# Kernel tuning notes

Hardware: AMD Instinct MI355X
Metric: run time of the kernel (lower is better)

The kernel has to match this reference:

```python
import jax, jax.numpy as jnp
from jax import lax
import numpy as np

B = 2048; IMG = 28; K = 3; CIN = 1; HC = 32; LC = 16; WID = 64; HID = 64
LIS = IMG - 3 * (K - 1)           # 22: latent image size
FLAT = LIS * LIS * HC             # 15488
BLK = WID * LC                    # 1024: hypernet block size
T1 = 10.0; T0 = 0.0; NSTEP = 20   # fixed-step RK4 replaces adaptive dopri5
VAR = 0.1                         # p_z0 diagonal covariance


def _conv(x, w, b):  # w: [Cout,Cin,k,k], VALID conv, stride 1
    y = lax.conv_general_dilated(x, w, (1, 1), 'VALID',
                                 dimension_numbers=('NCHW', 'OIHW', 'NCHW'))
    return y + b[None, :, None, None]


def _convT(x, w, b):  # w: [Cin,Cout,k,k] (pytorch ConvTranspose2d layout)
    wf = jnp.flip(w, (2, 3)).transpose(1, 0, 2, 3)  # -> OIHW, spatially flipped
    y = lax.conv_general_dilated(x, wf, (1, 1), [(K - 1, K - 1), (K - 1, K - 1)],
                                 dimension_numbers=('NCHW', 'OIHW', 'NCHW'))
    return y + b[None, :, None, None]


def _forward(x, c0w, c0b, c1w, c1b, c2w, c2b, elw, elb, dlw, dlb,
             t0w, t0b, t1w, t1b, t2w, t2b, h1w, h1b, h2w, h2b, h3w, h3b):
    # ---- encoder (dropout in eval = identity) ----
    h = jnp.tanh(_conv(x, c0w, c0b))
    h = jnp.tanh(_conv(h, c1w, c1b))
    h = jnp.tanh(_conv(h, c2w, c2b))
    z1 = h.reshape(h.shape[0], -1) @ elw + elb          # [B, LC]
    # ---- decoder ----
    d = jnp.tanh(z1 @ dlw + dlb)                         # [B, FLAT]
    d = d.reshape(-1, HC, LIS, LIS)
    d = jnp.tanh(_convT(d, t0w, t0b))
    d = jnp.tanh(_convT(d, t1w, t1b))
    recon = _convT(d, t2w, t2b)                          # [B, CIN, 28, 28]

    # ---- CNF vector field with analytic trace ----
    def hyper(t):
        p = jnp.tanh(jnp.reshape(jnp.asarray(t, jnp.float32), (1, 1)) @ h1w + h1b)
        p = jnp.tanh(p @ h2w + h2b)
        p = (p @ h3w + h3b).reshape(-1)
        W = p[:BLK].reshape(WID, LC)
        U = p[BLK:2 * BLK].reshape(WID, LC) * jax.nn.sigmoid(p[2 * BLK:3 * BLK].reshape(WID, LC))
        Bb = p[3 * BLK:]                                 # [WID]
        return W, Bb, U

    def f(t, z):
        W, Bb, U = hyper(t)
        hh = jnp.tanh(jnp.einsum('bd,wd->wb', z, W) + Bb[:, None])   # [WID, B]
        dz = jnp.einsum('wb,wd->bd', hh, U) / WID                     # [B, LC]
        s = jnp.sum(W * U, axis=1)                                    # [WID]: sum_i W_w[i]U_w[i]
        tr = jnp.mean((1.0 - hh * hh) * s[:, None], axis=0)           # [B] analytic trace
        return dz, -tr[:, None]

    dt = (T0 - T1) / NSTEP

    def step(state, i):
        z, lp = state
        t = T1 + i * dt
        k1z, k1l = f(t, z)
        k2z, k2l = f(t + 0.5 * dt, z + 0.5 * dt * k1z)
        k3z, k3l = f(t + 0.5 * dt, z + 0.5 * dt * k2z)
        k4z, k4l = f(t + dt, z + dt * k3z)
        z = z + dt / 6.0 * (k1z + 2 * k2z + 2 * k3z + k4z)
        lp = lp + dt / 6.0 * (k1l + 2 * k2l + 2 * k3l + k4l)
        return (z, lp), None

    lp1 = jnp.zeros((z1.shape[0], 1), z1.dtype)
    (z0, lp0), _ = lax.scan(step, (z1, lp1), jnp.arange(NSTEP, dtype=jnp.float32))

    # MultivariateNormal(0, 0.1*I) log_prob
    logp = -0.5 * (LC * jnp.log(2 * jnp.pi) + LC * jnp.log(VAR) + jnp.sum(z0 * z0, -1) / VAR)
    x_probs = jnp.mean(logp - lp0[:, 0])
    return recon, x_probs


def setup_inputs() -> dict:
    key = jax.random.key(0)
    ks = jax.random.split(key, 16)
    n = jax.random.normal
    s = jnp.float32(0.05)
    z = jnp.zeros
    OUT3 = 3 * BLK + WID
    return {
        'x': n(ks[0], (B, CIN, IMG, IMG), jnp.float32),
        'c0w': n(ks[1], (HC, CIN, K, K)) * s, 'c0b': z((HC,)),
        'c1w': n(ks[2], (HC, HC, K, K)) * s, 'c1b': z((HC,)),
        'c2w': n(ks[3], (HC, HC, K, K)) * s, 'c2b': z((HC,)),
        'elw': n(ks[4], (FLAT, LC)) * s, 'elb': z((LC,)),
        'dlw': n(ks[5], (LC, FLAT)) * s, 'dlb': z((FLAT,)),
        't0w': n(ks[6], (HC, HC, K, K)) * s, 't0b': z((HC,)),
        't1w': n(ks[7], (HC, HC, K, K)) * s, 't1b': z((HC,)),
        't2w': n(ks[8], (HC, CIN, K, K)) * s, 't2b': z((CIN,)),
        'h1w': n(ks[9], (1, HID)) * s, 'h1b': z((HID,)),
        'h2w': n(ks[10], (HID, HID)) * s, 'h2b': z((HID,)),
        'h3w': n(ks[11], (HID, OUT3)) * s, 'h3b': z((OUT3,)),
    }


def reference(x, c0w, c0b, c1w, c1b, c2w, c2b, elw, elb, dlw, dlb,
              t0w, t0b, t1w, t1b, t2w, t2b, h1w, h1b, h2w, h2b, h3w, h3b):
    return _forward(x, c0w, c0b, c1w, c1b, c2w, c2b, elw, elb, dlw, dlb,
                    t0w, t0b, t1w, t1b, t2w, t2b, h1w, h1b, h2w, h2b, h3w, h3b)
```

## Files before the change

### kernel.cpp

```cpp
#include <hip/hip_runtime.h>
#include <math.h>

#define Bsz 2048

using bf16x8 = __attribute__((ext_vector_type(8))) short;
using f32x4  = __attribute__((ext_vector_type(4))) float;

__device__ __forceinline__ float fast_tanh(float x){
    float e = __expf(2.0f * x);
    return 1.0f - 2.0f / (e + 1.0f);
}
__device__ __forceinline__ float fast_sigmoid(float x){
    return 1.0f / (1.0f + __expf(-x));
}
__device__ __forceinline__ unsigned short f2b(float f){
    union { float f; unsigned u; } v; v.f = f;
    unsigned r = v.u + 0x7FFFu + ((v.u >> 16) & 1u);
    return (unsigned short)(r >> 16);
}
__device__ __forceinline__ float b2f(unsigned short s){
    union { unsigned u; float f; } v; v.u = ((unsigned)s) << 16;
    return v.f;
}

__device__ __forceinline__ float stage_t(int sidx){
    int i  = sidx >> 2, st = sidx & 3;
    float t = 10.0f - 0.5f * (float)i;
    if (st == 1 || st == 2) t -= 0.25f;
    else if (st == 3)       t -= 0.5f;
    return t;
}

__global__ void k_prep(const float* __restrict__ c1w, const float* __restrict__ c2w,
                       const float* __restrict__ t0w, const float* __restrict__ t1w,
                       const float* __restrict__ elw, const float* __restrict__ dlw,
                       const float* __restrict__ elb, const float* __restrict__ dlb,
                       unsigned short* __restrict__ wc1, unsigned short* __restrict__ wc2,
                       unsigned short* __restrict__ wt0, unsigned short* __restrict__ wt1,
                       unsigned short* __restrict__ elwT, unsigned short* __restrict__ dlwT,
                       float* __restrict__ dlbT, float* __restrict__ z1, int full){
    int gsz = gridDim.x * 256;
    for (int i = blockIdx.x*256 + threadIdx.x; i < 9216; i += gsz){
        int ci = i & 31, co = (i >> 5) & 31, s = i >> 10;
        wc1[i] = f2b(c1w[(co*32 + ci)*9 + s]);
        wc2[i] = f2b(c2w[(co*32 + ci)*9 + s]);
        wt0[i] = f2b(t0w[(ci*32 + co)*9 + (8 - s)]);
        wt1[i] = f2b(t1w[(ci*32 + co)*9 + (8 - s)]);
    }
    if (!full) return;
    for (int i = blockIdx.x*256 + threadIdx.x; i < 32768; i += gsz)
        z1[i] = elb[i & 15];
    for (int i = blockIdx.x*256 + threadIdx.x; i < 15488; i += gsz){
        int pos = i >> 5, ci = i & 31;
        dlbT[i] = dlb[ci*484 + pos];
    }
    for (int i = blockIdx.x*256 + threadIdx.x; i < 247808; i += gsz){
        int l = i / 15488, f2 = i - l*15488;
        int pos = f2 >> 5, ci = f2 & 31;
        elwT[i] = f2b(elw[(ci*484 + pos)*16 + l]);
    }
    for (int i = blockIdx.x*256 + threadIdx.x; i < 247808; i += gsz){
        int f2 = i >> 4, l = i & 15;
        int pos = f2 >> 5, ci = f2 & 31;
        dlwT[i] = f2b(dlw[l*15488 + ci*484 + pos]);
    }
}

__global__ void __launch_bounds__(256)
k_enc01(const float* __restrict__ x, const float* __restrict__ c0w,
        const float* __restrict__ c0b, const unsigned short* __restrict__ wc1,
        const float* __restrict__ c1b, unsigned short* __restrict__ A1,
        int cb){
    __shared__ __align__(16) unsigned short A0L[676*40];
    const int tid = threadIdx.x, b = blockIdx.x;
    const float* xin = x + (size_t)(cb + b)*784;

    for (int pos = tid; pos < 676; pos += 256){
        int y = pos / 26, xx = pos - y*26;
        float v[9];
#pragma unroll
        for (int r = 0; r < 3; r++)
#pragma unroll
            for (int s = 0; s < 3; s++)
                v[r*3+s] = xin[(y+r)*28 + xx + s];
        unsigned short* ob = A0L + pos*40;
#pragma unroll
        for (int g = 0; g < 8; g++){
            float a0 = c0b[g*4+0], a1 = c0b[g*4+1], a2 = c0b[g*4+2], a3 = c0b[g*4+3];
#pragma unroll
            for (int k = 0; k < 9; k++){
                a0 += v[k] * c0w[(g*4+0)*9 + k];
                a1 += v[k] * c0w[(g*4+1)*9 + k];
                a2 += v[k] * c0w[(g*4+2)*9 + k];
                a3 += v[k] * c0w[(g*4+3)*9 + k];
            }
            ushort4 o;
            o.x = f2b(fast_tanh(a0)); o.y = f2b(fast_tanh(a1));
            o.z = f2b(fast_tanh(a2)); o.w = f2b(fast_tanh(a3));
            *(ushort4*)(ob + g*4) = o;
        }
    }
    __syncthreads();

    const int wave = tid >> 6, lane = tid & 63;
    const int q = lane >> 4, nn = lane & 15;
    bf16x8 af[2][9];
#pragma unroll
    for (int mt = 0; mt < 2; mt++)
#pragma unroll
        for (int s = 0; s < 9; s++)
            af[mt][s] = *(const bf16x8*)(wc1 + s*1024 + (mt*16 + nn)*32 + q*8);
    float4 bc0 = *(const float4*)(c1b + q*4);
    float4 bc1 = *(const float4*)(c1b + 16 + q*4);
    unsigned short* outb = A1 + (size_t)b*25088;

    for (int t = wave; t < 36; t += 4){
        int pos = t*16 + nn;
        int oy = pos / 24, ox = pos - oy*24;
        const unsigned short* ib = A0L + (oy*26 + ox)*40 + q*8;
        f32x4 acc0 = {0.f,0.f,0.f,0.f}, acc1 = {0.f,0.f,0.f,0.f};
#pragma unroll
        for (int r = 0; r < 3; r++){
            bf16x8 b0 = *(const bf16x8*)(ib + (r*26 + 0)*40);
            bf16x8 b1 = *(const bf16x8*)(ib + (r*26 + 1)*40);
            bf16x8 b2 = *(const bf16x8*)(ib + (r*26 + 2)*40);
            acc0 = __builtin_amdgcn_mfma_f32_16x16x32_bf16(af[0][r*3+0], b0, acc0, 0,0,0);
            acc1 = __builtin_amdgcn_mfma_f32_16x16x32_bf16(af[1][r*3+0], b0, acc1, 0,0,0);
            acc0 = __builtin_amdgcn_mfma_f32_16x16x32_bf16(af[0][r*3+1], b1, acc0, 0,0,0);
            acc1 = __builtin_amdgcn_mfma_f32_16x16x32_bf16(af[1][r*3+1], b1, acc1, 0,0,0);
            acc0 = __builtin_amdgcn_mfma_f32_16x16x32_bf16(af[0][r*3+2], b2, acc0, 0,0,0);
            acc1 = __builtin_amdgcn_mfma_f32_16x16x32_bf16(af[1][r*3+2], b2, acc1, 0,0,0);
        }
        int opix = oy*24 + ox;
        ushort4 o0, o1;
        o0.x = f2b(fast_tanh(acc0[0] + bc0.x)); o0.y = f2b(fast_tanh(acc0[1] + bc0.y));
        o0.z = f2b(fast_tanh(acc0[2] + bc0.z)); o0.w = f2b(fast_tanh(acc0[3] + bc0.w));
        o1.x = f2b(fast_tanh(acc1[0] + bc1.x)); o1.y = f2b(fast_tanh(acc1[1] + bc1.y));
        o1.z = f2b(fast_tanh(acc1[2] + bc1.z)); o1.w = f2b(fast_tanh(acc1[3] + bc1.w));
        *(ushort4*)(outb + opix*32 + q*4)      = o0;
        *(ushort4*)(outb + opix*32 + 16 + q*4) = o1;
    }
}

template<int IL, int OL, int OW, int OOFF, int INS, int OUTS>
__global__ void __launch_bounds__(256)
k_convM(const unsigned short* __restrict__ in, const unsigned short* __restrict__ wg,
        const float* __restrict__ bias, unsigned short* __restrict__ out, int CH){
    constexpr int N  = OL * OL;
    constexpr int NT = (N + 15) / 16;
    const int tid = threadIdx.x;
    const int wave = tid >> 6, lane = tid & 63;
    const int q = lane >> 4, nn = lane & 15;
    const int nw = gridDim.x * 4;

    bf16x8 af[2][9];
#pragma unroll
    for (int mt = 0; mt < 2; mt++)
#pragma unroll
        for (int s = 0; s < 9; s++)
            af[mt][s] = *(const bf16x8*)(wg + s*1024 + (mt*16 + nn)*32 + q*8);
    float4 bc0 = *(const float4*)(bias + q*4);
    float4 bc1 = *(const float4*)(bias + 16 + q*4);

    for (int t = blockIdx.x*4 + wave; t < CH*NT; t += nw){
        int img = t / NT, tt = t - img*NT;
        const unsigned short* inb = in + (size_t)img * INS;
        unsigned short* outb = out + (size_t)img * OUTS;
        int pos = tt*16 + nn;
        int pc  = pos < N ? pos : N - 1;
        int oy = pc / OL, ox = pc - oy*OL;
        const unsigned short* ib = inb + (oy*IL + ox)*32 + q*8;
        f32x4 acc0 = {0.f,0.f,0.f,0.f}, acc1 = {0.f,0.f,0.f,0.f};
#pragma unroll
        for (int r = 0; r < 3; r++){
            bf16x8 b0 = *(const bf16x8*)(ib + (r*IL + 0)*32);
            bf16x8 b1 = *(const bf16x8*)(ib + (r*IL + 1)*32);
            bf16x8 b2 = *(const bf16x8*)(ib + (r*IL + 2)*32);
            acc0 = __builtin_amdgcn_mfma_f32_16x16x32_bf16(af[0][r*3+0], b0, acc0, 0,0,0);
            acc1 = __builtin_amdgcn_mfma_f32_16x16x32_bf16(af[1][r*3+0], b0, acc1, 0,0,0);
            acc0 = __builtin_amdgcn_mfma_f32_16x16x32_bf16(af[0][r*3+1], b1, acc0, 0,0,0);
            acc1 = __builtin_amdgcn_mfma_f32_16x16x32_bf16(af[1][r*3+1], b1, acc1, 0,0,0);
            acc0 = __builtin_amdgcn_mfma_f32_16x16x32_bf16(af[0][r*3+2], b2, acc0, 0,0,0);
            acc1 = __builtin_amdgcn_mfma_f32_16x16x32_bf16(af[1][r*3+2], b2, acc1, 0,0,0);
        }
        if (pos < N){
            int opix = oy*OW + ox + OOFF;
            ushort4 o0, o1;
            o0.x = f2b(fast_tanh(acc0[0] + bc0.x)); o0.y = f2b(fast_tanh(acc0[1] + bc0.y));
            o0.z = f2b(fast_tanh(acc0[2] + bc0.z)); o0.w = f2b(fast_tanh(acc0[3] + bc0.w));
            o1.x = f2b(fast_tanh(acc1[0] + bc1.x)); o1.y = f2b(fast_tanh(acc1[1] + bc1.y));
            o1.z = f2b(fast_tanh(acc1[2] + bc1.z)); o1.w = f2b(fast_tanh(acc1[3] + bc1.w));
            *(ushort4*)(outb + opix*32 + q*4)      = o0;
            *(ushort4*)(outb + opix*32 + 16 + q*4) = o1;
        }
    }
}

__global__ void __launch_bounds__(256)
k_encg(const unsigned short* __restrict__ A2, const unsigned short* __restrict__ elwT,
       float* __restrict__ z1, int cb, int CH){
    int wave = threadIdx.x >> 6, lane = threadIdx.x & 63;
    int q = lane >> 4, nn = lane & 15;
    int imgb = blockIdx.x*16;
    const unsigned short* ap = A2 + (size_t)(imgb + nn)*15488 + q*8;
    const unsigned short* bp = elwT + (size_t)nn*15488 + q*8;
    f32x4 acc = {0.f,0.f,0.f,0.f};
    int s0 = blockIdx.y*121;
#pragma unroll 2
    for (int s = s0 + wave; s < s0 + 121; s += 4){
        bf16x8 a = *(const bf16x8*)(ap + s*32);
        bf16x8 b = *(const bf16x8*)(bp + s*32);
        acc = __builtin_amdgcn_mfma_f32_16x16x32_bf16(a, b, acc, 0,0,0);
    }
    float* zp = z1 + (size_t)(cb + imgb)*16;
#pragma unroll
    for (int i = 0; i < 4; i++)
        atomicAdd(zp + (q*4 + i)*16 + nn, acc[i]);
}

__global__ void __launch_bounds__(256)
k_dect0(const float* __restrict__ z1, const unsigned short* __restrict__ dlwT,
        const float* __restrict__ dlbT, const unsigned short* __restrict__ wt0,
        const float* __restrict__ t0b, unsigned short* __restrict__ D1, int cb){
    __shared__ __align__(16) unsigned short D0L[676*40];
    const int tid = threadIdx.x, b = blockIdx.x;
    unsigned short* d1b = D1 + (size_t)b*25088;

    {
        uint4 zq = {0,0,0,0};
        for (int p = tid; p < 676; p += 256){
            int y = p / 26, xx = p - y*26;
            if (y < 2 || y >= 24 || xx < 2 || xx >= 24){
                uint4* pt = (uint4*)(D0L + p*40);
                pt[0] = zq; pt[1] = zq; pt[2] = zq; pt[3] = zq;
            }
        }
        for (int p = tid; p < 784; p += 256){
            int y = p / 28, xx = p - y*28;
            if (y < 2 || y >= 26 || xx < 2 || xx >= 26){
                uint4* pt = (uint4*)(d1b + p*32);
                pt[0] = zq; pt[1] = zq; pt[2] = zq; pt[3] = zq;
            }
        }
    }
    float zz[16];
#pragma unroll
    for (int l = 0; l < 16; l++) zz[l] = z1[(size_t)(cb + b)*16 + l];
    {
        int ci = tid & 31, po = tid >> 5;
#pragma unroll 2
        for (int rr = 0; rr < 61; rr++){
            int pos = rr*8 + po;
            if (pos < 484){
                int y = pos / 22, xx = pos - y*22;
                const unsigned short* w = dlwT + (size_t)(pos*32 + ci)*16;
                bf16x8 w0 = *(const bf16x8*)(w);
                bf16x8 w1 = *(const bf16x8*)(w + 8);
                float a = dlbT[pos*32 + ci];
#pragma unroll
                for (int j = 0; j < 8; j++){
                    a += zz[j]     * b2f((unsigned short)w0[j]);
                    a += zz[8 + j] * b2f((unsigned short)w1[j]);
                }
                D0L[((y+2)*26 + xx + 2)*40 + ci] = f2b(fast_tanh(a));
            }
        }
    }
    __syncthreads();

    const int wave = tid >> 6, lane = tid & 63;
    const int q = lane >> 4, nn = lane & 15;
    bf16x8 af[2][9];
#pragma unroll
    for (int mt = 0; mt < 2; mt++)
#pragma unroll
        for (int s = 0; s < 9; s++)
            af[mt][s] = *(const bf16x8*)(wt0 + s*1024 + (mt*16 + nn)*32 + q*8);
    float4 bc0 = *(const float4*)(t0b + q*4);
    float4 bc1 = *(const float4*)(t0b + 16 + q*4);

    for (int t = wave; t < 36; t += 4){
        int pos = t*16 + nn;
        int oy = pos / 24, ox = pos - oy*24;
        const unsigned short* ib = D0L + (oy*26 + ox)*40 + q*8;
        f32x4 acc0 = {0.f,0.f,0.f,0.f}, acc1 = {0.f,0.f,0.f,0.f};
#pragma unroll
        for (int r = 0; r < 3; r++){
            bf16x8 b0 = *(const bf16x8*)(ib + (r*26 + 0)*40);
            bf16x8 b1 = *(const bf16x8*)(ib + (r*26 + 1)*40);
            bf16x8 b2 = *(const bf16x8*)(ib + (r*26 + 2)*40);
            acc0 = __builtin_amdgcn_mfma_f32_16x16x32_bf16(af[0][r*3+0], b0, acc0, 0,0,0);
            acc1 = __builtin_amdgcn_mfma_f32_16x16x32_bf16(af[1][r*3+0], b0, acc1, 0,0,0);
            acc0 = __builtin_amdgcn_mfma_f32_16x16x32_bf16(af[0][r*3+1], b1, acc0, 0,0,0);
            acc1 = __builtin_amdgcn_mfma_f32_16x16x32_bf16(af[1][r*3+1], b1, acc1, 0,0,0);
            acc0 = __builtin_amdgcn_mfma_f32_16x16x32_bf16(af[0][r*3+2], b2, acc0, 0,0,0);
            acc1 = __builtin_amdgcn_mfma_f32_16x16x32_bf16(af[1][r*3+2], b2, acc1, 0,0,0);
        }
        int opix = oy*28 + ox + 58;
        ushort4 o0, o1;
        o0.x = f2b(fast_tanh(acc0[0] + bc0.x)); o0.y = f2b(fast_tanh(acc0[1] + bc0.y));
        o0.z = f2b(fast_tanh(acc0[2] + bc0.z)); o0.w = f2b(fast_tanh(acc0[3] + bc0.w));
        o1.x = f2b(fast_tanh(acc1[0] + bc1.x)); o1.y = f2b(fast_tanh(acc1[1] + bc1.y));
        o1.z = f2b(fast_tanh(acc1[2] + bc1.z)); o1.w = f2b(fast_tanh(acc1[3] + bc1.w));
        *(ushort4*)(d1b + opix*32 + q*4)      = o0;
        *(ushort4*)(d1b + opix*32 + 16 + q*4) = o1;
    }
}

__global__ void __launch_bounds__(256)
k_dect12(const unsigned short* __restrict__ D1, const unsigned short* __restrict__ wt1,
         const float* __restrict__ t1b, const float* __restrict__ t2w,
         const float* __restrict__ t2b, float* __restrict__ out, int cb){
    __shared__ __align__(16) unsigned short D2L[676*40];
    const int tid = threadIdx.x, b = blockIdx.x;
    const unsigned short* d1b = D1 + (size_t)b*25088;
    const int wave = tid >> 6, lane = tid & 63;
    const int q = lane >> 4, nn = lane & 15;

    bf16x8 af[2][9];
#pragma unroll
    for (int mt = 0; mt < 2; mt++)
#pragma unroll
        for (int s = 0; s < 9; s++)
            af[mt][s] = *(const bf16x8*)(wt1 + s*1024 + (mt*16 + nn)*32 + q*8);
    float4 bc0 = *(const float4*)(t1b + q*4);
    float4 bc1 = *(const float4*)(t1b + 16 + q*4);

    for (int t = wave; t < 43; t += 4){
        int pos = t*16 + nn;
        int pc  = pos < 676 ? pos : 675;
        int oy = pc / 26, ox = pc - oy*26;
        const unsigned short* ib = d1b + (oy*28 + ox)*32 + q*8;
        f32x4 acc0 = {0.f,0.f,0.f,0.f}, acc1 = {0.f,0.f,0.f,0.f};
#pragma unroll
        for (int r = 0; r < 3; r++){
            bf16x8 b0 = *(const bf16x8*)(ib + (r*28 + 0)*32);
            bf16x8 b1 = *(const bf16x8*)(ib + (r*28 + 1)*32);
            bf16x8 b2 = *(const bf16x8*)(ib + (r*28 + 2)*32);
            acc0 = __builtin_amdgcn_mfma_f32_16x16x32_bf16(af[0][r*3+0], b0, acc0, 0,0,0);
            acc1 = __builtin_amdgcn_mfma_f32_16x16x32_bf16(af[1][r*3+0], b0, acc1, 0,0,0);
            acc0 = __builtin_amdgcn_mfma_f32_16x16x32_bf16(af[0][r*3+1], b1, acc0, 0,0,0);
            acc1 = __builtin_amdgcn_mfma_f32_16x16x32_bf16(af[1][r*3+1], b1, acc1, 0,0,0);
            acc0 = __builtin_amdgcn_mfma_f32_16x16x32_bf16(af[0][r*3+2], b2, acc0, 0,0,0);
            acc1 = __builtin_amdgcn_mfma_f32_16x16x32_bf16(af[1][r*3+2], b2, acc1, 0,0,0);
        }
        if (pos < 676){
            int opix = oy*26 + ox;
            ushort4 o0, o1;
            o0.x = f2b(fast_tanh(acc0[0] + bc0.x)); o0.y = f2b(fast_tanh(acc0[1] + bc0.y));
            o0.z = f2b(fast_tanh(acc0[2] + bc0.z)); o0.w = f2b(fast_tanh(acc0[3] + bc0.w));
            o1.x = f2b(fast_tanh(acc1[0] + bc1.x)); o1.y = f2b(fast_tanh(acc1[1] + bc1.y));
            o1.z = f2b(fast_tanh(acc1[2] + bc1.z)); o1.w = f2b(fast_tanh(acc1[3] + bc1.w));
            *(ushort4*)(D2L + opix*40 + q*4)      = o0;
            *(ushort4*)(D2L + opix*40 + 16 + q*4) = o1;
        }
    }
    __syncthreads();

    for (int o = tid; o < 784; o += 256){
        int y = o / 28, xx = o - y*28;
        float a = t2b[0];
#pragma unroll
        for (int r = 0; r < 3; r++){
            int iy = y + r - 2;
            if ((unsigned)iy >= 26u) continue;
#pragma unroll
            for (int s = 0; s < 3; s++){
                int ix = xx + s - 2;
                if ((unsigned)ix >= 26u) continue;
                const unsigned short* pp = D2L + (iy*26 + ix)*40;
                int wi = (2-r)*3 + (2-s);
#pragma unroll
                for (int g = 0; g < 4; g++){
                    bf16x8 h = *(const bf16x8*)(pp + g*8);
#pragma unroll
                    for (int j = 0; j < 8; j++)
                        a += b2f((unsigned short)h[j]) * t2w[(g*8+j)*9 + wi];
                }
            }
        }
        out[(size_t)(cb + b)*784 + o] = a;
    }
}

template<int LOUT, int INW, int OUTW, int OUTOFF>
__device__ __forceinline__ void conv_gemm(const unsigned short* __restrict__ Wg,
                                          const float* __restrict__ bias,
                                          const unsigned short* inL,
                                          unsigned short* outL, int tid){
    constexpr int N  = LOUT * LOUT;
    constexpr int NT = (N + 15) / 16;
    const int lane  = tid & 63;
    const int wave  = tid >> 6;
    const int mtile = wave & 1;
    const int quad  = lane >> 4;
    const int nn    = lane & 15;
    bf16x8 afr[9];
    const unsigned short* wp = Wg + (mtile*16 + nn)*32 + quad*8;
#pragma unroll
    for (int s = 0; s < 9; s++)
        afr[s] = *(const bf16x8*)(wp + s*1024);
    float4 bco = *(const float4*)(bias + mtile*16 + quad*4);
    for (int t = (wave >> 1); t < NT; t += 2){
        int pos = t*16 + nn;
        int pc  = pos < N ? pos : N - 1;
        int y = pc / LOUT, x = pc - y*LOUT;
        const unsigned short* ib = inL + (y*INW + x)*32 + quad*8;
        f32x4 acc = {0.f, 0.f, 0.f, 0.f};
#pragma unroll
        for (int r = 0; r < 3; r++)
#pragma unroll
            for (int s = 0; s < 3; s++)
                acc = __builtin_amdgcn_mfma_f32_16x16x32_bf16(
                        afr[r*3+s], *(const bf16x8*)(ib + (r*INW + s)*32), acc, 0, 0, 0);
        if (pos < N){
            ushort4 o;
            o.x = f2b(fast_tanh(acc[0] + bco.x));
            o.y = f2b(fast_tanh(acc[1] + bco.y));
            o.z = f2b(fast_tanh(acc[2] + bco.z));
            o.w = f2b(fast_tanh(acc[3] + bco.w));
            int opix = y*OUTW + x + OUTOFF;
            *(ushort4*)(outL + opix*32 + mtile*16 + quad*4) = o;
        }
    }
}

__global__ void __launch_bounds__(256)
k_enc_f(const float* __restrict__ x,
        const float* __restrict__ c0w, const float* __restrict__ c0b,
        const unsigned short* __restrict__ wc1, const float* __restrict__ c1b,
        const unsigned short* __restrict__ wc2, const float* __restrict__ c2b,
        const float* __restrict__ elw, const float* __restrict__ elb,
        float* __restrict__ z1){
    __shared__ float X[784];
    __shared__ __align__(16) unsigned short H0[21632];
    __shared__ __align__(16) unsigned short H1[18432];
    __shared__ __align__(16) unsigned short H2[15488];
    __shared__ float red[16*17];
    const int tid = threadIdx.x, b = blockIdx.x;
    for (int i = tid; i < 784; i += 256) X[i] = x[b*784 + i];
    __syncthreads();
    for (int pos = tid; pos < 676; pos += 256){
        int y = pos / 26, xx = pos - y*26;
        float v[9];
#pragma unroll
        for (int r = 0; r < 3; r++)
#pragma unroll
            for (int s = 0; s < 3; s++)
                v[r*3+s] = X[(y+r)*28 + xx + s];
#pragma unroll
        for (int g = 0; g < 8; g++){
            float a0 = c0b[g*4+0], a1 = c0b[g*4+1], a2 = c0b[g*4+2], a3 = c0b[g*4+3];
#pragma unroll
            for (int k = 0; k < 9; k++){
                a0 += v[k] * c0w[(g*4+0)*9 + k];
                a1 += v[k] * c0w[(g*4+1)*9 + k];
                a2 += v[k] * c0w[(g*4+2)*9 + k];
                a3 += v[k] * c0w[(g*4+3)*9 + k];
            }
            ushort4 o;
            o.x = f2b(fast_tanh(a0)); o.y = f2b(fast_tanh(a1));
            o.z = f2b(fast_tanh(a2)); o.w = f2b(fast_tanh(a3));
            *(ushort4*)(H0 + pos*32 + g*4) = o;
        }
    }
    __syncthreads();
    conv_gemm<24, 26, 24, 0>(wc1, c1b, H0, H1, tid);
    __syncthreads();
    conv_gemm<22, 24, 22, 0>(wc2, c2b, H1, H2, tid);
    __syncthreads();
    {
        int fg = tid >> 4, l = tid & 15;
        float a = 0.f;
        for (int ci = 0; ci < 32; ci++)
            for (int pos = fg; pos < 484; pos += 16)
                a += b2f(H2[pos*32 + ci]) * elw[(ci*484 + pos)*16 + l];
        red[fg*17 + l] = a;
        __syncthreads();
        if (tid < 16){
            float s = elb[tid];
#pragma unroll
            for (int g = 0; g < 16; g++) s += red[g*17 + tid];
            z1[b*16 + tid] = s;
        }
    }
}

__global__ void __launch_bounds__(256)
k_dec_f(const float* __restrict__ z1,
        const float* __restrict__ dlw, const float* __restrict__ dlb,
        const unsigned short* __restrict__ wt0, const float* __restrict__ t0b,
        const unsigned short* __restrict__ wt1, const float* __restrict__ t1b,
        const float* __restrict__ t2w, const float* __restrict__ t2b,
        float* __restrict__ out){
    __shared__ __align__(16) unsigned short D0[21632];
    __shared__ __align__(16) unsigned short D1[25088];
    __shared__ __align__(16) unsigned short D2[28800];
    const int tid = threadIdx.x, b = blockIdx.x;
    {
        uint4 zq = {0,0,0,0};
        for (int i = tid; i < 2704; i += 256) ((uint4*)D0)[i] = zq;
        for (int i = tid; i < 3136; i += 256) ((uint4*)D1)[i] = zq;
        for (int i = tid; i < 3600; i += 256) ((uint4*)D2)[i] = zq;
    }
    float zz[16];
#pragma unroll
    for (int l = 0; l < 16; l++) zz[l] = z1[b*16 + l];
    __syncthreads();
    for (int f = tid; f < 15488; f += 256){
        float a = dlb[f];
#pragma unroll
        for (int l = 0; l < 16; l++) a += zz[l] * dlw[l*15488 + f];
        int ci = f / 484, pos = f - ci*484;
        int y = pos / 22, xx = pos - y*22;
        D0[((y+2)*26 + xx + 2)*32 + ci] = f2b(fast_tanh(a));
    }
    __syncthreads();
    conv_gemm<24, 26, 28, 58>(wt0, t0b, D0, D1, tid);
    __syncthreads();
    conv_gemm<26, 28, 30, 62>(wt1, t1b, D1, D2, tid);
    __syncthreads();
    for (int o = tid; o < 784; o += 256){
        int y = o / 28, xx = o - y*28;
        float a = t2b[0];
#pragma unroll
        for (int r = 0; r < 3; r++)
#pragma unroll
            for (int s = 0; s < 3; s++){
                const unsigned short* pp = D2 + ((y+r)*30 + xx + s)*32;
                int wi = (2-r)*3 + (2-s);
#pragma unroll
                for (int g = 0; g < 4; g++){
                    bf16x8 h = *(const bf16x8*)(pp + g*8);
#pragma unroll
// ... 243 lines not shown
                lp[i] += (dt/6.f) * lacc[i];
                zsv = z[i];
                zacc[i] = 0.f; lacc[i] = 0.f;
            }
            zsb[(q*4 + i)*24 + d] = f2b(zsv);
        }
    }
    float sq[4];
#pragma unroll
    for (int i = 0; i < 4; i++) sq[i] = z[i]*z[i];
#pragma unroll
    for (int off = 1; off < 16; off <<= 1){
#pragma unroll
        for (int i = 0; i < 4; i++) sq[i] += __shfl_xor(sq[i], off, 16);
    }
    if (d == 0){
#pragma unroll
        for (int i = 0; i < 4; i++){
            float logp = -0.5f * (16.f*1.8378770664093453f
                                 + 16.f*(-2.302585092994046f) + sq[i]*10.f);
            part[blockIdx.x*16 + q*4 + i] = logp - lp[i];
        }
    }
}

struct PF { float4 Wr[4]; float4 Ur[4]; float Bb, sw; };
__device__ __forceinline__ void load_pf(const float* __restrict__ g,
                                        int lane, int q, int d, PF& p){
    const float4* w4 = (const float4*)(g + lane*16);
    p.Wr[0] = w4[0]; p.Wr[1] = w4[1]; p.Wr[2] = w4[2]; p.Wr[3] = w4[3];
    const float4* u4 = (const float4*)(g + 1024 + d*64 + q*16);
    p.Ur[0] = u4[0]; p.Ur[1] = u4[1]; p.Ur[2] = u4[2]; p.Ur[3] = u4[3];
    p.Bb = g[2048 + lane];
    p.sw = g[2112 + lane];
}
__global__ void __launch_bounds__(64)
k_cnf_f(const float* __restrict__ z1, const float* __restrict__ hyp,
        float* __restrict__ part){
    __shared__ __align__(16) float zsl[16];
    __shared__ __align__(16) float hhl[64];
    const int lane = threadIdx.x;
    const int q = lane >> 4, d = lane & 15;
    const float dt = -0.5f;
    float z  = z1[(size_t)blockIdx.x*16 + d];
    float zs = z;
    float lp = 0.f, zacc = 0.f, lacc = 0.f;
    if (lane < 16) zsl[lane] = zs;
    PF cur, nxt;
    load_pf(hyp, lane, q, d, cur);
    for (int sidx = 0; sidx < 80; sidx++){
        __syncthreads();
        if (sidx < 79) load_pf(hyp + (size_t)(sidx + 1)*2304, lane, q, d, nxt);
        const float4* zp = (const float4*)zsl;
        float4 z0 = zp[0], z1v = zp[1], z2 = zp[2], z3 = zp[3];
        float a = cur.Bb;
        a += z0.x*cur.Wr[0].x + z0.y*cur.Wr[0].y + z0.z*cur.Wr[0].z + z0.w*cur.Wr[0].w;
        a += z1v.x*cur.Wr[1].x + z1v.y*cur.Wr[1].y + z1v.z*cur.Wr[1].z + z1v.w*cur.Wr[1].w;
        a += z2.x*cur.Wr[2].x + z2.y*cur.Wr[2].y + z2.z*cur.Wr[2].z + z2.w*cur.Wr[2].w;
        a += z3.x*cur.Wr[3].x + z3.y*cur.Wr[3].y + z3.z*cur.Wr[3].z + z3.w*cur.Wr[3].w;
        float hh = fast_tanh(a);
        float e = (1.f - hh*hh) * cur.sw;
#pragma unroll
        for (int off = 1; off < 64; off <<= 1)
            e += __shfl_xor(e, off);
        hhl[lane] = hh;
        __syncthreads();
        const float4* hp = (const float4*)(hhl + q*16);
        float4 h0 = hp[0], h1 = hp[1], h2 = hp[2], h3 = hp[3];
        float dzp = 0.f;
        dzp += h0.x*cur.Ur[0].x + h0.y*cur.Ur[0].y + h0.z*cur.Ur[0].z + h0.w*cur.Ur[0].w;
        dzp += h1.x*cur.Ur[1].x + h1.y*cur.Ur[1].y + h1.z*cur.Ur[1].z + h1.w*cur.Ur[1].w;
        dzp += h2.x*cur.Ur[2].x + h2.y*cur.Ur[2].y + h2.z*cur.Ur[2].z + h2.w*cur.Ur[2].w;
        dzp += h3.x*cur.Ur[3].x + h3.y*cur.Ur[3].y + h3.z*cur.Ur[3].z + h3.w*cur.Ur[3].w;
        dzp += __shfl_xor(dzp, 16);
        dzp += __shfl_xor(dzp, 32);
        float dz = dzp * (1.f/64.f);
        float dl = -e  * (1.f/64.f);
        int st = sidx & 3;
        float wgt = (st == 0 || st == 3) ? 1.f : 2.f;
        zacc += wgt * dz;
        lacc += wgt * dl;
        if (st < 3){
            float aa = (st == 2) ? 1.0f : 0.5f;
            zs = z + aa * dt * dz;
        } else {
            z  += (dt/6.f) * zacc;
            lp += (dt/6.f) * lacc;
            zs = z;
            zacc = 0.f; lacc = 0.f;
        }
        if (lane < 16) zsl[lane] = zs;
        cur = nxt;
    }
    float sq = z * z;
#pragma unroll
    for (int off = 1; off < 16; off <<= 1) sq += __shfl_xor(sq, off, 16);
    float logp = -0.5f * (16.f*1.8378770664093453f + 16.f*(-2.302585092994046f) + sq*10.f);
    if (lane == 0) part[blockIdx.x] = logp - lp;
}

__global__ void k_final(const float* __restrict__ part, float* __restrict__ out){
    __shared__ float red[256];
    int tid = threadIdx.x;
    float s = 0.f;
#pragma unroll
    for (int k = 0; k < 8; k++) s += part[tid + k*256];
    red[tid] = s;
    __syncthreads();
    for (int st = 128; st > 0; st >>= 1){
        if (tid < st) red[tid] += red[tid + st];
        __syncthreads();
    }
    if (tid == 0) out[1605632] = red[0] * (1.f/2048.f);
}

extern "C" void kernel_launch(void* const* d_in, const int* in_sizes, int n_in,
                              void* d_out, int out_size, void* d_ws, size_t ws_size,
                              hipStream_t stream){
    const float* x   = (const float*)d_in[0];
    const float* c0w = (const float*)d_in[1];
    const float* c0b = (const float*)d_in[2];
    const float* c1w = (const float*)d_in[3];
    const float* c1b = (const float*)d_in[4];
    const float* c2w = (const float*)d_in[5];
    const float* c2b = (const float*)d_in[6];
    const float* elw = (const float*)d_in[7];
    const float* elb = (const float*)d_in[8];
    const float* dlw = (const float*)d_in[9];
    const float* dlb = (const float*)d_in[10];
    const float* t0w = (const float*)d_in[11];
    const float* t0b = (const float*)d_in[12];
    const float* t1w = (const float*)d_in[13];
    const float* t1b = (const float*)d_in[14];
    const float* t2w = (const float*)d_in[15];
    const float* t2b = (const float*)d_in[16];
    const float* h1w = (const float*)d_in[17];
    const float* h1b = (const float*)d_in[18];
    const float* h2w = (const float*)d_in[19];
    const float* h2b = (const float*)d_in[20];
    const float* h3w = (const float*)d_in[21];
    const float* h3b = (const float*)d_in[22];

    float* ws   = (float*)d_ws;
    float* z1   = ws;
    float* hyp  = z1 + 32768;
    float* part = hyp + 184320;
    float* p2ws = part + 2048;
    float* p3ws = p2ws + 5120;
    float* dlbT = p3ws + 256000;
    unsigned short* wc1  = (unsigned short*)(dlbT + 15488);
    unsigned short* wc2  = wc1 + 9216;
    unsigned short* wt0  = wc2 + 9216;
    unsigned short* wt1  = wt0 + 9216;
    unsigned short* elwT = wt1 + 9216;
    unsigned short* dlwT = elwT + 247808;
    unsigned short* act  = dlwT + 247808;
    float* rec  = (float*)d_out;

    const size_t MISC = 3047936;
    int CH = 0;
    const int cands[6] = {2048, 1024, 512, 256, 128, 64};
    for (int c = 0; c < 6; c++){
        size_t need = MISC + (size_t)cands[c] * 81152;
        if (need <= ws_size){ CH = cands[c]; break; }
    }

    if (CH == 0){
        k_hyper<<<80, 256, 0, stream>>>(h1w, h1b, h2w, h2b, h3w, h3b, hyp);
        k_prep <<<64,   256, 0, stream>>>(c1w, c2w, t0w, t1w, elw, dlw, elb, dlb,
                                          wc1, wc2, wt0, wt1, wt1, wt1, z1, z1, 0);
        k_enc_f<<<2048, 256, 0, stream>>>(x, c0w, c0b, wc1, c1b, wc2, c2b, elw, elb, z1);
        k_cnf_f<<<2048,  64, 0, stream>>>(z1, hyp, part);
        k_dec_f<<<2048, 256, 0, stream>>>(z1, dlw, dlb, wt0, t0b, wt1, t1b, t2w, t2b, rec);
        k_final<<<1,    256, 0, stream>>>(part, rec);
        return;
    }

    k_hyp1<<<80,           64, 0, stream>>>(h1w, h1b, h2w, h2b, p2ws);
    k_hyp2<<<dim3(13,80), 256, 0, stream>>>(p2ws, h3w, h3b, p3ws);
    k_hyp3<<<80,          256, 0, stream>>>(p3ws, hyp);

    k_prep<<<64, 256, 0, stream>>>(c1w, c2w, t0w, t1w, elw, dlw, elb, dlb,
                                   wc1, wc2, wt0, wt1, elwT, dlwT, dlbT, z1, 1);

    unsigned short* X = act;
    unsigned short* Y = X + (size_t)CH*25088;

    for (int cb = 0; cb < Bsz; cb += CH){
        k_enc01<<<CH, 256, 0, stream>>>(x, c0w, c0b, wc1, c1b, X, cb);
        k_convM<24,22,22,0, 25088, 15488><<<(CH*31 + 15)/16, 256, 0, stream>>>(X, wc2, c2b, Y, CH);
        k_encg<<<dim3(CH/16, 4), 256, 0, stream>>>(Y, elwT, z1, cb, CH);
        k_dect0<<<CH, 256, 0, stream>>>(z1, dlwT, dlbT, wt0, t0b, X, cb);
        k_dect12<<<CH, 256, 0, stream>>>(X, wt1, t1b, t2w, t2b, rec, cb);
    }
    k_cnfM <<<128,  64, 0, stream>>>(z1, hyp, part);
    k_final<<<1,   256, 0, stream>>>(part, rec);
}
```

Before: 653.8 us.

## Move decoder linear and final transposed conv onto MFMA, split decoder linear

The decoder's dense z1@dlw layer moves out of the per-image k_dect0 scalar loop into a new batched MFMA kernel (k_decgM). It writes bf16 activations into the spare Y buffer, which k_dect0 then copies into shared memory. The last transposed conv in k_dect12 becomes a padded-LDS MFMA over 9 taps using bf16-packed t2w weights, replacing the scalar per-pixel loop. The first encoder conv is also restructured to reuse the input taps across all 32 outputs. This adds a kernel launch and a global round trip for the decoder activations, and lowers the final conv to bf16 weights.

```diff
diff --git a/kernel.cpp b/kernel.cpp
--- a/kernel.cpp
+++ b/kernel.cpp
@@ -35,8 +35,10 @@
                        const float* __restrict__ t0w, const float* __restrict__ t1w,
                        const float* __restrict__ elw, const float* __restrict__ dlw,
                        const float* __restrict__ elb, const float* __restrict__ dlb,
+                       const float* __restrict__ t2w,
                        unsigned short* __restrict__ wc1, unsigned short* __restrict__ wc2,
                        unsigned short* __restrict__ wt0, unsigned short* __restrict__ wt1,
+                       unsigned short* __restrict__ t2wPk,
                        unsigned short* __restrict__ elwT, unsigned short* __restrict__ dlwT,
                        float* __restrict__ dlbT, float* __restrict__ z1, int full){
     int gsz = gridDim.x * 256;
@@ -48,6 +50,11 @@
         wt1[i] = f2b(t1w[(ci*32 + co)*9 + (8 - s)]);
     }
     if (!full) return;
+    for (int i = blockIdx.x*256 + threadIdx.x; i < 288; i += gsz){
+        int tap = i >> 5, ci = i & 31;
+        int r = tap / 3, s = tap - r*3;
+        t2wPk[i] = f2b(t2w[ci*9 + (2-r)*3 + (2-s)]);
+    }
     for (int i = blockIdx.x*256 + threadIdx.x; i < 32768; i += gsz)
         z1[i] = elb[i & 15];
     for (int i = blockIdx.x*256 + threadIdx.x; i < 15488; i += gsz){
@@ -83,20 +90,20 @@
 #pragma unroll
             for (int s = 0; s < 3; s++)
                 v[r*3+s] = xin[(y+r)*28 + xx + s];
+        float acc[32];
+#pragma unroll
+        for (int co = 0; co < 32; co++) acc[co] = c0b[co];
+#pragma unroll
+        for (int k = 0; k < 9; k++)
+#pragma unroll
+            for (int co = 0; co < 32; co++)
+                acc[co] += v[k] * c0w[co*9 + k];
         unsigned short* ob = A0L + pos*40;
 #pragma unroll
         for (int g = 0; g < 8; g++){
-            float a0 = c0b[g*4+0], a1 = c0b[g*4+1], a2 = c0b[g*4+2], a3 = c0b[g*4+3];
-#pragma unroll
-            for (int k = 0; k < 9; k++){
-                a0 += v[k] * c0w[(g*4+0)*9 + k];
-                a1 += v[k] * c0w[(g*4+1)*9 + k];
-                a2 += v[k] * c0w[(g*4+2)*9 + k];
-                a3 += v[k] * c0w[(g*4+3)*9 + k];
-            }
             ushort4 o;
-            o.x = f2b(fast_tanh(a0)); o.y = f2b(fast_tanh(a1));
-            o.z = f2b(fast_tanh(a2)); o.w = f2b(fast_tanh(a3));
+            o.x = f2b(fast_tanh(acc[g*4+0])); o.y = f2b(fast_tanh(acc[g*4+1]));
+            o.z = f2b(fast_tanh(acc[g*4+2])); o.w = f2b(fast_tanh(acc[g*4+3]));
             *(ushort4*)(ob + g*4) = o;
         }
     }
@@ -219,9 +226,49 @@
 }
 
 __global__ void __launch_bounds__(256)
-k_dect0(const float* __restrict__ z1, const unsigned short* __restrict__ dlwT,
-        const float* __restrict__ dlbT, const unsigned short* __restrict__ wt0,
-        const float* __restrict__ t0b, unsigned short* __restrict__ D1, int cb){
+k_decgM(const float* __restrict__ z1, const unsigned short* __restrict__ dlwT,
+        const float* __restrict__ dlbT, unsigned short* __restrict__ D0c, int cb){
+    __shared__ float zb[16*17];
+    const int tid = threadIdx.x;
+    const int wave = tid >> 6, lane = tid & 63;
+    const int q = lane >> 4, n = lane & 15;
+    const int imgb = blockIdx.y*16;
+    zb[(tid >> 4)*17 + (tid & 15)] = z1[(size_t)(cb + imgb + (tid >> 4))*16 + (tid & 15)];
+    __syncthreads();
+
+    bf16x8 zf;
+    if (q < 2){
+        unsigned short tmp[8];
+#pragma unroll
+        for (int j = 0; j < 8; j++) tmp[j] = f2b(zb[n*17 + q*8 + j]);
+        zf = *(bf16x8*)tmp;
+    } else {
+        bf16x8 zz = {0,0,0,0,0,0,0,0}; zf = zz;
+    }
+
+#pragma unroll
+    for (int ii = 0; ii < 4; ii++){
+        int mt = blockIdx.x*16 + wave*4 + ii;
+        if (mt >= 968) break;
+        int mb = mt*16;
+        bf16x8 afr;
+        if (q < 2) afr = *(const bf16x8*)(dlwT + (size_t)(mb + n)*16 + q*8);
+        else { bf16x8 zz = {0,0,0,0,0,0,0,0}; afr = zz; }
+        f32x4 acc = {0.f,0.f,0.f,0.f};
+        acc = __builtin_amdgcn_mfma_f32_16x16x32_bf16(afr, zf, acc, 0,0,0);
+        float4 bias = *(const float4*)(dlbT + mb + q*4);
+        ushort4 o;
+        o.x = f2b(fast_tanh(acc[0] + bias.x));
+        o.y = f2b(fast_tanh(acc[1] + bias.y));
+        o.z = f2b(fast_tanh(acc[2] + bias.z));
+        o.w = f2b(fast_tanh(acc[3] + bias.w));
+        *(ushort4*)(D0c + (size_t)(imgb + n)*15488 + mb + q*4) = o;
+    }
+}
+
+__global__ void __launch_bounds__(256)
+k_dect0(const unsigned short* __restrict__ D0c, const unsigned short* __restrict__ wt0,
+        const float* __restrict__ t0b, unsigned short* __restrict__ D1){
     __shared__ __align__(16) unsigned short D0L[676*40];
     const int tid = threadIdx.x, b = blockIdx.x;
     unsigned short* d1b = D1 + (size_t)b*25088;
@@ -243,27 +290,13 @@
             }
         }
     }
-    float zz[16];
-#pragma unroll
-    for (int l = 0; l < 16; l++) zz[l] = z1[(size_t)(cb + b)*16 + l];
     {
-        int ci = tid & 31, po = tid >> 5;
-#pragma unroll 2
-        for (int rr = 0; rr < 61; rr++){
-            int pos = rr*8 + po;
-            if (pos < 484){
-                int y = pos / 22, xx = pos - y*22;
-                const unsigned short* w = dlwT + (size_t)(pos*32 + ci)*16;
-                bf16x8 w0 = *(const bf16x8*)(w);
-                bf16x8 w1 = *(const bf16x8*)(w + 8);
-                float a = dlbT[pos*32 + ci];
-#pragma unroll
-                for (int j = 0; j < 8; j++){
-                    a += zz[j]     * b2f((unsigned short)w0[j]);
-                    a += zz[8 + j] * b2f((unsigned short)w1[j]);
-                }
-                D0L[((y+2)*26 + xx + 2)*40 + ci] = f2b(fast_tanh(a));
-            }
+        const uint4* src = (const uint4*)(D0c + (size_t)b*15488);
+        for (int c = tid; c < 1936; c += 256){
+            uint4 v = src[c];
+            int pos = c >> 2, p8 = (c & 3)*8;
+            int y = pos / 22, xx = pos - y*22;
+            *(uint4*)(D0L + ((y+2)*26 + xx + 2)*40 + p8) = v;
         }
     }
     __syncthreads();
@@ -309,77 +342,89 @@
 
 __global__ void __launch_bounds__(256)
 k_dect12(const unsigned short* __restrict__ D1, const unsigned short* __restrict__ wt1,
-         const float* __restrict__ t1b, const float* __restrict__ t2w,
+         const float* __restrict__ t1b, const unsigned short* __restrict__ t2wPk,
          const float* __restrict__ t2b, float* __restrict__ out, int cb){
-    __shared__ __align__(16) unsigned short D2L[676*40];
+    __shared__ __align__(16) unsigned short D2L[900*40];
     const int tid = threadIdx.x, b = blockIdx.x;
     const unsigned short* d1b = D1 + (size_t)b*25088;
     const int wave = tid >> 6, lane = tid & 63;
     const int q = lane >> 4, nn = lane & 15;
 
-    bf16x8 af[2][9];
-#pragma unroll
-    for (int mt = 0; mt < 2; mt++)
-#pragma unroll
-        for (int s = 0; s < 9; s++)
-            af[mt][s] = *(const bf16x8*)(wt1 + s*1024 + (mt*16 + nn)*32 + q*8);
-    float4 bc0 = *(const float4*)(t1b + q*4);
-    float4 bc1 = *(const float4*)(t1b + 16 + q*4);
-
-    for (int t = wave; t < 43; t += 4){
-        int pos = t*16 + nn;
-        int pc  = pos < 676 ? pos : 675;
-        int oy = pc / 26, ox = pc - oy*26;
-        const unsigned short* ib = d1b + (oy*28 + ox)*32 + q*8;
-        f32x4 acc0 = {0.f,0.f,0.f,0.f}, acc1 = {0.f,0.f,0.f,0.f};
-#pragma unroll
-        for (int r = 0; r < 3; r++){
-            bf16x8 b0 = *(const bf16x8*)(ib + (r*28 + 0)*32);
-            bf16x8 b1 = *(const bf16x8*)(ib + (r*28 + 1)*32);
-            bf16x8 b2 = *(const bf16x8*)(ib + (r*28 + 2)*32);
-            acc0 = __builtin_amdgcn_mfma_f32_16x16x32_bf16(af[0][r*3+0], b0, acc0, 0,0,0);
-            acc1 = __builtin_amdgcn_mfma_f32_16x16x32_bf16(af[1][r*3+0], b0, acc1, 0,0,0);
-            acc0 = __builtin_amdgcn_mfma_f32_16x16x32_bf16(af[0][r*3+1], b1, acc0, 0,0,0);
-            acc1 = __builtin_amdgcn_mfma_f32_16x16x32_bf16(af[1][r*3+1], b1, acc1, 0,0,0);
-            acc0 = __builtin_amdgcn_mfma_f32_16x16x32_bf16(af[0][r*3+2], b2, acc0, 0,0,0);
-            acc1 = __builtin_amdgcn_mfma_f32_16x16x32_bf16(af[1][r*3+2], b2, acc1, 0,0,0);
-        }
-        if (pos < 676){
-            int opix = oy*26 + ox;
-            ushort4 o0, o1;
-            o0.x = f2b(fast_tanh(acc0[0] + bc0.x)); o0.y = f2b(fast_tanh(acc0[1] + bc0.y));
-            o0.z = f2b(fast_tanh(acc0[2] + bc0.z)); o0.w = f2b(fast_tanh(acc0[3] + bc0.w));
-            o1.x = f2b(fast_tanh(acc1[0] + bc1.x)); o1.y = f2b(fast_tanh(acc1[1] + bc1.y));
-            o1.z = f2b(fast_tanh(acc1[2] + bc1.z)); o1.w = f2b(fast_tanh(acc1[3] + bc1.w));
-            *(ushort4*)(D2L + opix*40 + q*4)      = o0;
-            *(ushort4*)(D2L + opix*40 + 16 + q*4) = o1;
-        }
-    }
-    __syncthreads();
-
-    for (int o = tid; o < 784; o += 256){
-        int y = o / 28, xx = o - y*28;
-        float a = t2b[0];
-#pragma unroll
-        for (int r = 0; r < 3; r++){
-            int iy = y + r - 2;
-            if ((unsigned)iy >= 26u) continue;
-#pragma unroll
-            for (int s = 0; s < 3; s++){
-                int ix = xx + s - 2;
-                if ((unsigned)ix >= 26u) continue;
-                const unsigned short* pp = D2L + (iy*26 + ix)*40;
-                int wi = (2-r)*3 + (2-s);
-#pragma unroll
-                for (int g = 0; g < 4; g++){
-                    bf16x8 h = *(const bf16x8*)(pp + g*8);
-#pragma unroll
-                    for (int j = 0; j < 8; j++)
-                        a += b2f((unsigned short)h[j]) * t2w[(g*8+j)*9 + wi];
-                }
+    {
+        uint4 zq = {0,0,0,0};
+        for (int p = tid; p < 900; p += 256){
+            int y = p / 30, xx = p - y*30;
+            if (y < 2 || y >= 28 || xx < 2 || xx >= 28){
+                uint4* pt = (uint4*)(D2L + p*40);
+                pt[0] = zq; pt[1] = zq; pt[2] = zq; pt[3] = zq;
             }
         }
-        out[(size_t)(cb + b)*784 + o] = a;
+    }
+    {
+        bf16x8 af[2][9];
+#pragma unroll
+        for (int mt = 0; mt < 2; mt++)
+#pragma unroll
+            for (int s = 0; s < 9; s++)
+                af[mt][s] = *(const bf16x8*)(wt1 + s*1024 + (mt*16 + nn)*32 + q*8);
+        float4 bc0 = *(const float4*)(t1b + q*4);
+        float4 bc1 = *(const float4*)(t1b + 16 + q*4);
+
+        for (int t = wave; t < 43; t += 4){
+            int pos = t*16 + nn;
+            int pc  = pos < 676 ? pos : 675;
+            int oy = pc / 26, ox = pc - oy*26;
+            const unsigned short* ib = d1b + (oy*28 + ox)*32 + q*8;
+            f32x4 acc0 = {0.f,0.f,0.f,0.f}, acc1 = {0.f,0.f,0.f,0.f};
+#pragma unroll
+            for (int r = 0; r < 3; r++){
+                bf16x8 b0 = *(const bf16x8*)(ib + (r*28 + 0)*32);
+                bf16x8 b1 = *(const bf16x8*)(ib + (r*28 + 1)*32);
+                bf16x8 b2 = *(const bf16x8*)(ib + (r*28 + 2)*32);
+                acc0 = __builtin_amdgcn_mfma_f32_16x16x32_bf16(af[0][r*3+0], b0, acc0, 0,0,0);
+                acc1 = __builtin_amdgcn_mfma_f32_16x16x32_bf16(af[1][r*3+0], b0, acc1, 0,0,0);
+                acc0 = __builtin_amdgcn_mfma_f32_16x16x32_bf16(af[0][r*3+1], b1, acc0, 0,0,0);
+                acc1 = __builtin_amdgcn_mfma_f32_16x16x32_bf16(af[1][r*3+1], b1, acc1, 0,0,0);
+                acc0 = __builtin_amdgcn_mfma_f32_16x16x32_bf16(af[0][r*3+2], b2, acc0, 0,0,0);
+                acc1 = __builtin_amdgcn_mfma_f32_16x16x32_bf16(af[1][r*3+2], b2, acc1, 0,0,0);
+            }
+            if (pos < 676){
+                int opix = (oy + 2)*30 + ox + 2;
+                ushort4 o0, o1;
+                o0.x = f2b(fast_tanh(acc0[0] + bc0.x)); o0.y = f2b(fast_tanh(acc0[1] + bc0.y));
+                o0.z = f2b(fast_tanh(acc0[2] + bc0.z)); o0.w = f2b(fast_tanh(acc0[3] + bc0.w));
+                o1.x = f2b(fast_tanh(acc1[0] + bc1.x)); o1.y = f2b(fast_tanh(acc1[1] + bc1.y));
+                o1.z = f2b(fast_tanh(acc1[2] + bc1.z)); o1.w = f2b(fast_tanh(acc1[3] + bc1.w));
+                *(ushort4*)(D2L + opix*40 + q*4)      = o0;
+                *(ushort4*)(D2L + opix*40 + 16 + q*4) = o1;
+            }
+        }
+    }
+    __syncthreads();
+
+    {
+        bf16x8 wf[9];
+#pragma unroll
+        for (int tap = 0; tap < 9; tap++)
+            wf[tap] = *(const bf16x8*)(t2wPk + tap*32 + q*8);
+        float t2b0 = t2b[0];
+        for (int t = wave; t < 49; t += 4){
+            int p = t*16 + nn;
+            int y = p / 28, xx = p - y*28;
+            const unsigned short* bbase = D2L + (y*30 + xx)*40 + q*8;
+            f32x4 acc = {0.f,0.f,0.f,0.f};
+#pragma unroll
+            for (int r = 0; r < 3; r++){
+                acc = __builtin_amdgcn_mfma_f32_16x16x32_bf16(wf[r*3+0],
+                        *(const bf16x8*)(bbase + (r*30 + 0)*40), acc, 0,0,0);
+                acc = __builtin_amdgcn_mfma_f32_16x16x32_bf16(wf[r*3+1],
+                        *(const bf16x8*)(bbase + (r*30 + 1)*40), acc, 0,0,0);
+                acc = __builtin_amdgcn_mfma_f32_16x16x32_bf16(wf[r*3+2],
+                        *(const bf16x8*)(bbase + (r*30 + 2)*40), acc, 0,0,0);
+            }
+            if (q == 0)
+                out[(size_t)(cb + b)*784 + p] = acc[0] + t2b0;
+        }
     }
 }
 
@@ -929,12 +974,13 @@
     unsigned short* wc2  = wc1 + 9216;
     unsigned short* wt0  = wc2 + 9216;
     unsigned short* wt1  = wt0 + 9216;
-    unsigned short* elwT = wt1 + 9216;
+    unsigned short* t2wPk = wt1 + 9216;
+    unsigned short* elwT = t2wPk + 288;
     unsigned short* dlwT = elwT + 247808;
     unsigned short* act  = dlwT + 247808;
     float* rec  = (float*)d_out;
 
-    const size_t MISC = 3047936;
+    const size_t MISC = 3048512;
     int CH = 0;
     const int cands[6] = {2048, 1024, 512, 256, 128, 64};
     for (int c = 0; c < 6; c++){
@@ -944,8 +990,8 @@
 
     if (CH == 0){
         k_hyper<<<80, 256, 0, stream>>>(h1w, h1b, h2w, h2b, h3w, h3b, hyp);
-        k_prep <<<64,   256, 0, stream>>>(c1w, c2w, t0w, t1w, elw, dlw, elb, dlb,
-                                          wc1, wc2, wt0, wt1, wt1, wt1, z1, z1, 0);
+        k_prep <<<64,   256, 0, stream>>>(c1w, c2w, t0w, t1w, elw, dlw, elb, dlb, t2w,
+                                          wc1, wc2, wt0, wt1, t2wPk, wt1, wt1, z1, z1, 0);
         k_enc_f<<<2048, 256, 0, stream>>>(x, c0w, c0b, wc1, c1b, wc2, c2b, elw, elb, z1);
         k_cnf_f<<<2048,  64, 0, stream>>>(z1, hyp, part);
         k_dec_f<<<2048, 256, 0, stream>>>(z1, dlw, dlb, wt0, t0b, wt1, t1b, t2w, t2b, rec);
@@ -957,8 +1003,8 @@
     k_hyp2<<<dim3(13,80), 256, 0, stream>>>(p2ws, h3w, h3b, p3ws);
     k_hyp3<<<80,          256, 0, stream>>>(p3ws, hyp);
 
-    k_prep<<<64, 256, 0, stream>>>(c1w, c2w, t0w, t1w, elw, dlw, elb, dlb,
-                                   wc1, wc2, wt0, wt1, elwT, dlwT, dlbT, z1, 1);
+    k_prep<<<64, 256, 0, stream>>>(c1w, c2w, t0w, t1w, elw, dlw, elb, dlb, t2w,
+                                   wc1, wc2, wt0, wt1, t2wPk, elwT, dlwT, dlbT, z1, 1);
 
     unsigned short* X = act;
     unsigned short* Y = X + (size_t)CH*25088;
@@ -967,8 +1013,9 @@
         k_enc01<<<CH, 256, 0, stream>>>(x, c0w, c0b, wc1, c1b, X, cb);
         k_convM<24,22,22,0, 25088, 15488><<<(CH*31 + 15)/16, 256, 0, stream>>>(X, wc2, c2b, Y, CH);
         k_encg<<<dim3(CH/16, 4), 256, 0, stream>>>(Y, elwT, z1, cb, CH);
-        k_dect0<<<CH, 256, 0, stream>>>(z1, dlwT, dlbT, wt0, t0b, X, cb);
-        k_dect12<<<CH, 256, 0, stream>>>(X, wt1, t1b, t2w, t2b, rec, cb);
+        k_decgM<<<dim3(61, CH/16), 256, 0, stream>>>(z1, dlwT, dlbT, Y, cb);
+        k_dect0<<<CH, 256, 0, stream>>>(Y, wt0, t0b, X);
+        k_dect12<<<CH, 256, 0, stream>>>(X, wt1, t1b, t2wPk, t2b, rec, cb);
     }
     k_cnfM <<<128,  64, 0, stream>>>(z1, hyp, part);
     k_final<<<1,   256, 0, stream>>>(part, rec);
```

After: 583.7 us. 10.7% less time.
